# Kernel tuning notes

Hardware: AMD Instinct MI355X
Metric: run time of the kernel (lower is better)

Reference implementation:

```python
import jax, jax.numpy as jnp
import numpy as np

B, C, D, N, K = 2, 64, 3, 4096, 16
E = 2 * C      # edge-feature channels (128)
H = 2 * E      # expansion hidden channels (256)


def setup_inputs() -> dict:
    key = jax.random.key(0)
    ks = jax.random.split(key, 7)
    s1 = 1.0 / np.sqrt(E).astype(np.float32)
    s2 = 1.0 / np.sqrt(H).astype(np.float32)
    return {
        "x":  jax.random.normal(ks[0], (B, C, D, N), jnp.float32),
        "W1": jax.random.normal(ks[1], (H, E), jnp.float32) * s1,
        "b1": jax.random.normal(ks[2], (H,), jnp.float32) * s1,
        "W2": jax.random.normal(ks[3], (H, H), jnp.float32) * s2,
        "b2": jax.random.normal(ks[4], (H,), jnp.float32) * s2,
        "W3": jax.random.normal(ks[5], (C, H), jnp.float32) * s2,
        "b3": jax.random.normal(ks[6], (C,), jnp.float32) * s2,
    }


def _knn_idx(pc, k):
    """pc: (B, C, N). Returns (B, k, N) indices of k nearest neighbors
    (self excluded), matching KNN(ref=pc, query=pc) then idx[:, 1:, :]."""
    sq = jnp.sum(pc * pc, axis=1)                                  # (B, N)
    d2 = sq[:, :, None] - 2.0 * jnp.einsum('bcn,bcm->bnm', pc, pc) + sq[:, None, :]
    _, idx = jax.lax.top_k(-d2, k + 1)                             # (B, N, k+1) nearest-first
    return jnp.transpose(idx[:, :, 1:], (0, 2, 1))                 # drop self -> (B, k, N)


def reference(x, W1, b1, W2, b2, W3, b3):
    mean_pc = jnp.mean(x, axis=2)                                  # (B, C, N)
    idx = _knn_idx(mean_pc, K)                                     # (B, K, N), int32
    # grouping_operation: out[b,c,k,n] = mean_pc[b, c, idx[b,k,n]]
    nbr = jax.vmap(lambda f, i: f[:, i])(mean_pc, idx)             # (B, C, K, N)
    central = jnp.broadcast_to(x[:, :, None, :, :], (B, C, K, D, N))
    nbr_e = jnp.broadcast_to(nbr[:, :, :, None, :], (B, C, K, D, N))
    edge = jnp.concatenate([central, nbr_e - central], axis=1)     # (B, 2C, K, D, N)
    bc = lambda b: b[None, :, None, None, None]
    h = jax.nn.relu(jnp.einsum('oi,bikdn->bokdn', W1, edge) + bc(b1))
    h = jax.nn.relu(jnp.einsum('oi,bikdn->bokdn', W2, h) + bc(b2))
    r = jnp.einsum('oi,bikdn->bokdn', W3, h) + bc(b3)              # (B, C, K, D, N)
    return jnp.max(r, axis=2) + x                                  # (B, C, D, N)
```

## Files before the change

kernel.cpp:

```cpp
#include <hip/hip_runtime.h>

typedef unsigned short u16;
typedef float f32x4 __attribute__((ext_vector_type(4)));
typedef short bf16x8 __attribute__((ext_vector_type(8)));
typedef u16 u16x4 __attribute__((ext_vector_type(4)));
typedef unsigned int uint2v __attribute__((ext_vector_type(2)));


static __device__ __forceinline__ u16 f2bf(float x) {
    union { float f; unsigned int u; } v; v.f = x;
    unsigned int u = v.u;
    unsigned int r = u + 0x7fffu + ((u >> 16) & 1u);
    return (u16)(r >> 16);
}

static __device__ __forceinline__ float bf2f(u16 h) {
    union { unsigned int u; float f; } v; v.u = ((unsigned int)h) << 16;
    return v.f;
}

static __device__ __forceinline__ unsigned int pk2(float a, float b) {
    return (unsigned int)f2bf(a) | ((unsigned int)f2bf(b) << 16);
}

__global__ __launch_bounds__(256) void mean_kernel(const float* __restrict__ x,
                                                   float* __restrict__ pc,
                                                   const float* __restrict__ W1,
                                                   const float* __restrict__ W2,
                                                   const float* __restrict__ W3,
                                                   u16* __restrict__ W2bf,
                                                   u16* __restrict__ W3bf,
                                                   float* __restrict__ W1dT,
                                                   float* __restrict__ W1bT) {
    int t = blockIdx.x * 256 + threadIdx.x;
    int n = t & 4095;
    int bc = t >> 12;
    const float* xp = x + bc * 3 * 4096 + n;
    pc[t] = (xp[0] + xp[4096] + xp[8192]) / 3.0f;

    if (t < 65536) {
        W2bf[t] = f2bf(W2[t]);
        if (t < 16384) {
            W3bf[t] = f2bf(W3[t]);
            int c = t >> 8, h = t & 255;
            float wa = W1[h * 128 + c];
            float wb = W1[h * 128 + 64 + c];
            W1dT[t] = wa - wb;
            W1bT[t] = wb;
        }
    }
}

#define INSERT(dist, idxv) do { \
    float _v = (dist); int _vi = (idxv); \
    _Pragma("unroll") \
    for (int _s = 0; _s < 16; ++_s) { \
        bool _c = _v < bd[_s]; \
        float _nb = _c ? _v : bd[_s]; \
        float _nv = _c ? bd[_s] : _v; \
        int _nbi = _c ? _vi : bi[_s]; \
        int _nvi = _c ? bi[_s] : _vi; \
        bd[_s] = _nb; _v = _nv; bi[_s] = _nbi; _vi = _nvi; \
    } } while (0)

__global__ __launch_bounds__(256, 3) void knn_part_kernel(const float* __restrict__ pc,
                                                          float* __restrict__ pd,
                                                          int* __restrict__ pi) {
    __shared__ float ptile[64][128];
    __shared__ float sqt[128];
    int tid = threadIdx.x;
    int bid = blockIdx.x;
    int ch = bid & 31, qb = (bid >> 5) & 15, b = bid >> 9;
    int n = qb * 256 + tid;
    int m0 = ch * 128;

    #pragma unroll
    for (int it = 0; it < 8; ++it) {
        int lin4 = it * 256 + tid;
        int c = lin4 >> 5, mm4 = (lin4 & 31) * 4;
        *(float4*)&ptile[c][mm4] =
            *(const float4*)&pc[(b * 64 + c) * 4096 + m0 + mm4];
    }
    __syncthreads();
    if (tid < 128) {
        float s = 0.f;
        #pragma unroll
        for (int c = 0; c < 64; ++c) {
            float v = ptile[c][tid];
            s = fmaf(v, v, s);
        }
        sqt[tid] = s;
    }

    float qv[64];
    float sqn = 0.f;
    #pragma unroll
    for (int c = 0; c < 64; ++c) {
        qv[c] = pc[(b * 64 + c) * 4096 + n];
        sqn = fmaf(qv[c], qv[c], sqn);
    }

    float bd[16]; int bi[16];
    #pragma unroll
    for (int s = 0; s < 16; ++s) { bd[s] = 3.4e38f; bi[s] = -1; }
    __syncthreads();

    for (int mb = 0; mb < 128; mb += 4) {
        float d0 = 0.f, d1 = 0.f, d2 = 0.f, d3 = 0.f;
        #pragma unroll
        for (int c = 0; c < 64; ++c) {
            float4 pv = *(const float4*)&ptile[c][mb];
            float qc = qv[c];
            d0 = fmaf(qc, pv.x, d0);
            d1 = fmaf(qc, pv.y, d1);
            d2 = fmaf(qc, pv.z, d2);
            d3 = fmaf(qc, pv.w, d3);
        }
        int m = m0 + mb;
        float e0 = (sqn - 2.f * d0) + sqt[mb + 0]; if (m + 0 == n) e0 = 3.4e38f;
        float e1 = (sqn - 2.f * d1) + sqt[mb + 1]; if (m + 1 == n) e1 = 3.4e38f;
        float e2 = (sqn - 2.f * d2) + sqt[mb + 2]; if (m + 2 == n) e2 = 3.4e38f;
        float e3 = (sqn - 2.f * d3) + sqt[mb + 3]; if (m + 3 == n) e3 = 3.4e38f;
        INSERT(e0, m + 0);
        INSERT(e1, m + 1);
        INSERT(e2, m + 2);
        INSERT(e3, m + 3);
    }
    int base = ((b * 4096 + n) * 32 + ch) * 16;
    #pragma unroll
    for (int s = 0; s < 16; ++s) { pd[base + s] = bd[s]; pi[base + s] = bi[s]; }
}

__global__ __launch_bounds__(256) void knn_merge_kernel(const float* __restrict__ pd,
                                                        const int* __restrict__ pi,
                                                        int* __restrict__ idxw) {
    int tid = threadIdx.x;
    int lane = tid & 63;
    int q = blockIdx.x * 4 + (tid >> 6);
    int base = q * 512;

    float d[8]; int ix[8];
    #pragma unroll
    for (int j = 0; j < 8; ++j) {
        d[j] = pd[base + lane + 64 * j];
        ix[j] = pi[base + lane + 64 * j];
    }

    for (int e = 0; e < 16; ++e) {
        float lmd = d[0]; int lmi = ix[0];
        #pragma unroll
        for (int j = 1; j < 8; ++j) {
            bool c = d[j] < lmd;
            lmd = c ? d[j] : lmd;
            lmi = c ? ix[j] : lmi;
        }
        float wm = lmd;
        #pragma unroll
        for (int off = 32; off; off >>= 1)
            wm = fminf(wm, __shfl_xor(wm, off));
        unsigned long long msk = __ballot(lmd == wm);
        int L = (int)__ffsll(msk) - 1;
        int wmi = __shfl(lmi, L);
        if (lane == 0) idxw[q * 16 + e] = wmi;
        if (lane == L) {
            #pragma unroll
            for (int j = 0; j < 8; ++j)
                if (ix[j] == wmi) d[j] = 3.4e38f;
        }
    }
}

__global__ __launch_bounds__(256) void qp_kernel(const float* __restrict__ pc,
                                                 const float* __restrict__ x,
                                                 const float* __restrict__ W1bT,
                                                 const float* __restrict__ W1dT,
                                                 const float* __restrict__ b1,
                                                 u16* __restrict__ Qbf,
                                                 u16* __restrict__ Pbf) {
    int h = threadIdx.x;
    int bid = blockIdx.x;
    if (bid < 1024) {
        int b = bid >> 9, m0 = (bid & 511) * 8;
        float a0 = 0.f, a1 = 0.f, a2 = 0.f, a3 = 0.f;
        float a4 = 0.f, a5 = 0.f, a6 = 0.f, a7 = 0.f;
        for (int c = 0; c < 64; ++c) {
            float w = W1bT[c * 256 + h];
            const float* pr = pc + (b * 64 + c) * 4096 + m0;
            float4 p0 = *(const float4*)pr;
            float4 p1 = *(const float4*)(pr + 4);
            a0 = fmaf(w, p0.x, a0); a1 = fmaf(w, p0.y, a1);
            a2 = fmaf(w, p0.z, a2); a3 = fmaf(w, p0.w, a3);
            a4 = fmaf(w, p1.x, a4); a5 = fmaf(w, p1.y, a5);
            a6 = fmaf(w, p1.z, a6); a7 = fmaf(w, p1.w, a7);
        }
        int ob = (b * 4096 + m0) * 256 + h;
        Qbf[ob] = f2bf(a0); Qbf[ob + 256] = f2bf(a1);
        Qbf[ob + 512] = f2bf(a2); Qbf[ob + 768] = f2bf(a3);
        Qbf[ob + 1024] = f2bf(a4); Qbf[ob + 1280] = f2bf(a5);
        Qbf[ob + 1536] = f2bf(a6); Qbf[ob + 1792] = f2bf(a7);
    } else {
        int pb = bid - 1024;
        int b = pb / 1536;
        int rem = pb % 1536;
        int d = rem >> 9;
        int n0 = (rem & 511) * 8;
        float bias = b1[h];
        float a0 = bias, a1 = bias, a2 = bias, a3 = bias;
        float a4 = bias, a5 = bias, a6 = bias, a7 = bias;
        for (int c = 0; c < 64; ++c) {
            float w = W1dT[c * 256 + h];
            const float* xr = x + ((b * 64 + c) * 3 + d) * 4096 + n0;
            float4 x0 = *(const float4*)xr;
            float4 x1 = *(const float4*)(xr + 4);
            a0 = fmaf(w, x0.x, a0); a1 = fmaf(w, x0.y, a1);
            a2 = fmaf(w, x0.z, a2); a3 = fmaf(w, x0.w, a3);
            a4 = fmaf(w, x1.x, a4); a5 = fmaf(w, x1.y, a5);
            a6 = fmaf(w, x1.z, a6); a7 = fmaf(w, x1.w, a7);
        }
        int ob = ((b * 3 + d) * 4096 + n0) * 256 + h;
        Pbf[ob] = f2bf(a0); Pbf[ob + 256] = f2bf(a1);
        Pbf[ob + 512] = f2bf(a2); Pbf[ob + 768] = f2bf(a3);
        Pbf[ob + 1024] = f2bf(a4); Pbf[ob + 1280] = f2bf(a5);
        Pbf[ob + 1536] = f2bf(a6); Pbf[ob + 1792] = f2bf(a7);
    }
}

__global__ __launch_bounds__(512) void fused_mlp_kernel(const float* __restrict__ x,
                                                        const u16* __restrict__ Pbf,
                                                        const u16* __restrict__ Qbf,
                                                        const int* __restrict__ idxw,
                                                        const u16* __restrict__ W2bf,
                                                        const u16* __restrict__ W3bf,
                                                        const float* __restrict__ b2,
                                                        const float* __restrict__ b3,
                                                        float* __restrict__ out) {
    __shared__ u16 hL[96][264];

    int tid = threadIdx.x;
    int bid = blockIdx.x;
    int b = bid >> 11;
    int rr = bid & 2047;
    int n0 = (((rr & 7) << 8) | (rr >> 3)) << 1;

    int w = tid >> 6, lane = tid & 63;
    int cl = lane & 15, q = lane >> 4;

    {
        int g = w & 1, kh = (w >> 1) * 4;
        int n = n0 + g;
        u16x4 pv[3];
        #pragma unroll
        for (int d = 0; d < 3; ++d)
            pv[d] = *(const u16x4*)&Pbf[((b * 3 + d) * 4096 + n) * 256 + lane * 4];
        const int* idq = idxw + (b * 4096 + n) * 16 + kh;
        #pragma unroll
        for (int kk = 0; kk < 4; ++kk) {
            int m = idq[kk];
            u16x4 qv = *(const u16x4*)&Qbf[(b * 4096 + m) * 256 + lane * 4];
            float q0 = bf2f(qv[0]), q1 = bf2f(qv[1]), q2 = bf2f(qv[2]), q3 = bf2f(qv[3]);
            #pragma unroll
            for (int d = 0; d < 3; ++d) {
                uint2v hv;
                hv[0] = pk2(fmaxf(bf2f(pv[d][0]) + q0, 0.f), fmaxf(bf2f(pv[d][1]) + q1, 0.f));
                hv[1] = pk2(fmaxf(bf2f(pv[d][2]) + q2, 0.f), fmaxf(bf2f(pv[d][3]) + q3, 0.f));
                *(uint2v*)&hL[g * 48 + d * 16 + kh + kk][lane * 4] = hv;
            }
        }
    }
    __syncthreads();

    f32x4 acc[2][6];
    #pragma unroll
    for (int i = 0; i < 2; ++i)
        #pragma unroll
        for (int jt = 0; jt < 6; ++jt)
            acc[i][jt] = (f32x4){0.f, 0.f, 0.f, 0.f};

    const u16* Arow = W2bf + (w * 32 + cl) * 256 + q * 8;
    for (int kt = 0; kt < 8; ++kt) {
        int k0 = kt * 32;
        bf16x8 a[2], bb[6];
        #pragma unroll
        for (int i = 0; i < 2; ++i)
            a[i] = *(const bf16x8*)(Arow + i * 4096 + k0);
        #pragma unroll
        for (int jt = 0; jt < 6; ++jt)
            bb[jt] = *(const bf16x8*)(&hL[jt * 16 + cl][k0 + q * 8]);
        #pragma unroll
        for (int i = 0; i < 2; ++i)
            #pragma unroll
            for (int jt = 0; jt < 6; ++jt)
                acc[i][jt] = __builtin_amdgcn_mfma_f32_16x16x32_bf16(a[i], bb[jt], acc[i][jt], 0, 0, 0);
    }
    __syncthreads();

    #pragma unroll
    for (int i = 0; i < 2; ++i) {
        int rowb = w * 32 + i * 16 + q * 4;
        float4 bv = *(const float4*)(b2 + rowb);
        #pragma unroll
        for (int jt = 0; jt < 6; ++jt) {
            f32x4 v = acc[i][jt];
            uint2v hv;
            hv[0] = pk2(fmaxf(v[0] + bv.x, 0.f), fmaxf(v[1] + bv.y, 0.f));
            hv[1] = pk2(fmaxf(v[2] + bv.z, 0.f), fmaxf(v[3] + bv.w, 0.f));
            *(uint2v*)&hL[jt * 16 + cl][rowb] = hv;
        }
    }
    __syncthreads();

    int rw = (w & 3) * 16, jt0 = (w >> 2) * 3;
    f32x4 acc3[3];
    #pragma unroll
    for (int jt = 0; jt < 3; ++jt) acc3[jt] = (f32x4){0.f, 0.f, 0.f, 0.f};

    const u16* A3row = W3bf + (rw + cl) * 256 + q * 8;
    for (int kt = 0; kt < 8; ++kt) {
        int k0 = kt * 32;
        bf16x8 a3 = *(const bf16x8*)(A3row + k0);
        #pragma unroll
        for (int jt = 0; jt < 3; ++jt) {
            bf16x8 bb = *(const bf16x8*)(&hL[(jt0 + jt) * 16 + cl][k0 + q * 8]);
            acc3[jt] = __builtin_amdgcn_mfma_f32_16x16x32_bf16(a3, bb, acc3[jt], 0, 0, 0);
        }
    }

    int rowb = rw + q * 4;
    float4 b3v = *(const float4*)(b3 + rowb);
    #pragma unroll
    for (int jt = 0; jt < 3; ++jt) {
        int jj = jt0 + jt;
        int g = jj / 3, d = jj % 3;
        int n = n0 + g;
        f32x4 v = acc3[jt];
        v[0] += b3v.x;
        v[1] += b3v.y;
        v[2] += b3v.z;
        v[3] += b3v.w;
        #pragma unroll
        for (int off = 1; off < 16; off <<= 1) {
            v[0] = fmaxf(v[0], __shfl_xor(v[0], off));
            v[1] = fmaxf(v[1], __shfl_xor(v[1], off));
            v[2] = fmaxf(v[2], __shfl_xor(v[2], off));
            v[3] = fmaxf(v[3], __shfl_xor(v[3], off));
        }
        if (cl == 0) {
            #pragma unroll
            for (int r = 0; r < 4; ++r) {
                int addr = ((b * 64 + rowb + r) * 3 + d) * 4096 + n;
                out[addr] = v[r] + x[addr];
            }
        }
    }
}

extern "C" void kernel_launch(void* const* d_in, const int* in_sizes, int n_in,
                              void* d_out, int out_size, void* d_ws, size_t ws_size,
                              hipStream_t stream) {
    (void)in_sizes; (void)n_in; (void)out_size; (void)ws_size;
    const float* x  = (const float*)d_in[0];
    const float* W1 = (const float*)d_in[1];
    const float* b1 = (const float*)d_in[2];
    const float* W2 = (const float*)d_in[3];
    const float* b2 = (const float*)d_in[4];
    const float* W3 = (const float*)d_in[5];
    const float* b3 = (const float*)d_in[6];
    float* out = (float*)d_out;

    char* ws = (char*)d_ws;
    float* pc   = (float*)(ws + 0);
    int*   idxw = (int*)  (ws + 2129920);
    u16*   Qbf  = (u16*)  (ws + 2654208);
    u16*   Pbf  = (u16*)  (ws + 6848512);
    u16*   W2bf = (u16*)  (ws + 19431424);
    u16*   W3bf = (u16*)  (ws + 19562496);
    float* W1dT = (float*)(ws + 19595264);
    float* W1bT = (float*)(ws + 19660800);
    float* pd   = (float*)(ws + 2654208);
    int*   pi   = (int*)  (ws + 19726336);

    mean_kernel<<<2048, 256, 0, stream>>>(x, pc, W1, W2, W3, W2bf, W3bf, W1dT, W1bT);
    knn_part_kernel<<<1024, 256, 0, stream>>>(pc, pd, pi);
    knn_merge_kernel<<<2048, 256, 0, stream>>>(pd, pi, idxw);
    qp_kernel<<<4096, 256, 0, stream>>>(pc, x, W1bT, W1dT, b1, Qbf, Pbf);
    fused_mlp_kernel<<<4096, 512, 0, stream>>>(x, Pbf, Qbf, idxw, W2bf, W3bf, b2, b3, out);
}
```

Before: 338.0 us.

## Compute first-layer projections with bf16 MFMA and retile the second GEMM

Replaces the scalar FMA qp kernel with an MFMA-based bf16 kernel, with bf16 copies of x, the mean point cloud and the transposed W1 halves produced in the mean kernel. The KNN partial indices are stored as 16-bit to cut the partial-result traffic. The fused MLP's W2 GEMM is retiled from 2x6 to 4x3 MFMA tiles per wave, which changes the balance between A-operand global loads and B-operand LDS loads. Quantising x and pc to bf16 before the first layer adds rounding error, and the mean kernel now writes extra data.

```diff
diff --git a/kernel.cpp b/kernel.cpp
--- a/kernel.cpp
+++ b/kernel.cpp
@@ -30,13 +30,22 @@
                                                    const float* __restrict__ W3,
                                                    u16* __restrict__ W2bf,
                                                    u16* __restrict__ W3bf,
-                                                   float* __restrict__ W1dT,
-                                                   float* __restrict__ W1bT) {
+                                                   u16* __restrict__ W1dTbf,
+                                                   u16* __restrict__ W1bTbf,
+                                                   u16* __restrict__ xbf,
+                                                   u16* __restrict__ pcbf) {
     int t = blockIdx.x * 256 + threadIdx.x;
     int n = t & 4095;
     int bc = t >> 12;
     const float* xp = x + bc * 3 * 4096 + n;
-    pc[t] = (xp[0] + xp[4096] + xp[8192]) / 3.0f;
+    float x0 = xp[0], x1 = xp[4096], x2 = xp[8192];
+    float m = (x0 + x1 + x2) / 3.0f;
+    pc[t] = m;
+    pcbf[t] = f2bf(m);
+    int xb = bc * 3 * 4096 + n;
+    xbf[xb] = f2bf(x0);
+    xbf[xb + 4096] = f2bf(x1);
+    xbf[xb + 8192] = f2bf(x2);
 
     if (t < 65536) {
         W2bf[t] = f2bf(W2[t]);
@@ -45,8 +54,8 @@
             int c = t >> 8, h = t & 255;
             float wa = W1[h * 128 + c];
             float wb = W1[h * 128 + 64 + c];
-            W1dT[t] = wa - wb;
-            W1bT[t] = wb;
+            W1dTbf[h * 64 + c] = f2bf(wa - wb);
+            W1bTbf[h * 64 + c] = f2bf(wb);
         }
     }
 }
@@ -65,7 +74,7 @@
 
 __global__ __launch_bounds__(256, 3) void knn_part_kernel(const float* __restrict__ pc,
                                                           float* __restrict__ pd,
-                                                          int* __restrict__ pi) {
+                                                          u16* __restrict__ pi) {
     __shared__ float ptile[64][128];
     __shared__ float sqt[128];
     int tid = threadIdx.x;
@@ -102,7 +111,7 @@
 
     float bd[16]; int bi[16];
     #pragma unroll
-    for (int s = 0; s < 16; ++s) { bd[s] = 3.4e38f; bi[s] = -1; }
+    for (int s = 0; s < 16; ++s) { bd[s] = 3.4e38f; bi[s] = 0; }
     __syncthreads();
 
     for (int mb = 0; mb < 128; mb += 4) {
@@ -128,11 +137,11 @@
     }
     int base = ((b * 4096 + n) * 32 + ch) * 16;
     #pragma unroll
-    for (int s = 0; s < 16; ++s) { pd[base + s] = bd[s]; pi[base + s] = bi[s]; }
+    for (int s = 0; s < 16; ++s) { pd[base + s] = bd[s]; pi[base + s] = (u16)bi[s]; }
 }
 
 __global__ __launch_bounds__(256) void knn_merge_kernel(const float* __restrict__ pd,
-                                                        const int* __restrict__ pi,
+                                                        const u16* __restrict__ pi,
                                                         int* __restrict__ idxw) {
     int tid = threadIdx.x;
     int lane = tid & 63;
@@ -143,7 +152,7 @@
     #pragma unroll
     for (int j = 0; j < 8; ++j) {
         d[j] = pd[base + lane + 64 * j];
-        ix[j] = pi[base + lane + 64 * j];
+        ix[j] = (int)pi[base + lane + 64 * j];
     }
 
     for (int e = 0; e < 16; ++e) {
@@ -170,58 +179,69 @@
     }
 }
 
-__global__ __launch_bounds__(256) void qp_kernel(const float* __restrict__ pc,
-                                                 const float* __restrict__ x,
-                                                 const float* __restrict__ W1bT,
-                                                 const float* __restrict__ W1dT,
-                                                 const float* __restrict__ b1,
-                                                 u16* __restrict__ Qbf,
-                                                 u16* __restrict__ Pbf) {
-    int h = threadIdx.x;
-    int bid = blockIdx.x;
-    if (bid < 1024) {
-        int b = bid >> 9, m0 = (bid & 511) * 8;
-        float a0 = 0.f, a1 = 0.f, a2 = 0.f, a3 = 0.f;
-        float a4 = 0.f, a5 = 0.f, a6 = 0.f, a7 = 0.f;
-        for (int c = 0; c < 64; ++c) {
-            float w = W1bT[c * 256 + h];
-            const float* pr = pc + (b * 64 + c) * 4096 + m0;
-            float4 p0 = *(const float4*)pr;
-            float4 p1 = *(const float4*)(pr + 4);
-            a0 = fmaf(w, p0.x, a0); a1 = fmaf(w, p0.y, a1);
-            a2 = fmaf(w, p0.z, a2); a3 = fmaf(w, p0.w, a3);
-            a4 = fmaf(w, p1.x, a4); a5 = fmaf(w, p1.y, a5);
-            a6 = fmaf(w, p1.z, a6); a7 = fmaf(w, p1.w, a7);
-        }
-        int ob = (b * 4096 + m0) * 256 + h;
-        Qbf[ob] = f2bf(a0); Qbf[ob + 256] = f2bf(a1);
-        Qbf[ob + 512] = f2bf(a2); Qbf[ob + 768] = f2bf(a3);
-        Qbf[ob + 1024] = f2bf(a4); Qbf[ob + 1280] = f2bf(a5);
-        Qbf[ob + 1536] = f2bf(a6); Qbf[ob + 1792] = f2bf(a7);
+__global__ __launch_bounds__(256) void qp_mfma_kernel(const u16* __restrict__ xbf,
+                                                      const u16* __restrict__ pcbf,
+                                                      const u16* __restrict__ W1dTbf,
+                                                      const u16* __restrict__ W1bTbf,
+                                                      const float* __restrict__ b1,
+                                                      u16* __restrict__ Qbf,
+                                                      u16* __restrict__ Pbf) {
+    int tid = threadIdx.x, bid = blockIdx.x;
+    int w = tid >> 6, lane = tid & 63, cl = lane & 15, q = lane >> 4;
+
+    const u16* Wt;
+    const u16* src;
+    u16* dst;
+    int cstride;
+    bool isP;
+    if (bid < 128) {
+        int lin = bid * 64;
+        int b = lin >> 12, m0 = lin & 4095;
+        Wt = W1bTbf;
+        dst = Qbf + (b * 4096 + m0) * 256;
+        src = pcbf + b * 64 * 4096 + m0;
+        cstride = 4096;
+        isP = false;
     } else {
-        int pb = bid - 1024;
-        int b = pb / 1536;
-        int rem = pb % 1536;
-        int d = rem >> 9;
-        int n0 = (rem & 511) * 8;
-        float bias = b1[h];
-        float a0 = bias, a1 = bias, a2 = bias, a3 = bias;
-        float a4 = bias, a5 = bias, a6 = bias, a7 = bias;
-        for (int c = 0; c < 64; ++c) {
-            float w = W1dT[c * 256 + h];
-            const float* xr = x + ((b * 64 + c) * 3 + d) * 4096 + n0;
-            float4 x0 = *(const float4*)xr;
-            float4 x1 = *(const float4*)(xr + 4);
-            a0 = fmaf(w, x0.x, a0); a1 = fmaf(w, x0.y, a1);
-            a2 = fmaf(w, x0.z, a2); a3 = fmaf(w, x0.w, a3);
-            a4 = fmaf(w, x1.x, a4); a5 = fmaf(w, x1.y, a5);
-            a6 = fmaf(w, x1.z, a6); a7 = fmaf(w, x1.w, a7);
-        }
-        int ob = ((b * 3 + d) * 4096 + n0) * 256 + h;
-        Pbf[ob] = f2bf(a0); Pbf[ob + 256] = f2bf(a1);
-        Pbf[ob + 512] = f2bf(a2); Pbf[ob + 768] = f2bf(a3);
-        Pbf[ob + 1024] = f2bf(a4); Pbf[ob + 1280] = f2bf(a5);
-        Pbf[ob + 1536] = f2bf(a6); Pbf[ob + 1792] = f2bf(a7);
+        int lin = (bid - 128) * 64;
+        int b = lin / 12288;
+        int r = lin % 12288;
+        int d = r >> 12, n0 = r & 4095;
+        Wt = W1dTbf;
+        dst = Pbf + ((b * 3 + d) * 4096 + n0) * 256;
+        src = xbf + ((b * 64) * 3 + d) * 4096 + n0;
+        cstride = 3 * 4096;
+        isP = true;
+    }
+    int cw = w * 16;
+
+    bf16x8 bfr[2];
+    #pragma unroll
+    for (int kh = 0; kh < 2; ++kh)
+        #pragma unroll
+        for (int j = 0; j < 8; ++j) {
+            int c = kh * 32 + q * 8 + j;
+            bfr[kh][j] = (short)src[c * cstride + cw + cl];
+        }
+
+    #pragma unroll
+    for (int ht = 0; ht < 16; ++ht) {
+        f32x4 acc = (f32x4){0.f, 0.f, 0.f, 0.f};
+        const u16* arow = Wt + (ht * 16 + cl) * 64 + q * 8;
+        bf16x8 a0 = *(const bf16x8*)arow;
+        bf16x8 a1 = *(const bf16x8*)(arow + 32);
+        acc = __builtin_amdgcn_mfma_f32_16x16x32_bf16(a0, bfr[0], acc, 0, 0, 0);
+        acc = __builtin_amdgcn_mfma_f32_16x16x32_bf16(a1, bfr[1], acc, 0, 0, 0);
+        u16x4 o;
+        if (isP) {
+            float4 bv = *(const float4*)(b1 + ht * 16 + q * 4);
+            o[0] = f2bf(acc[0] + bv.x); o[1] = f2bf(acc[1] + bv.y);
+            o[2] = f2bf(acc[2] + bv.z); o[3] = f2bf(acc[3] + bv.w);
+        } else {
+            o[0] = f2bf(acc[0]); o[1] = f2bf(acc[1]);
+            o[2] = f2bf(acc[2]); o[3] = f2bf(acc[3]);
+        }
+        *(u16x4*)&dst[(cw + cl) * 256 + ht * 16 + q * 4] = o;
     }
 }
 
@@ -269,42 +289,43 @@
     }
     __syncthreads();
 
-    f32x4 acc[2][6];
-    #pragma unroll
-    for (int i = 0; i < 2; ++i)
-        #pragma unroll
-        for (int jt = 0; jt < 6; ++jt)
+    int rowg = w & 3, colh = w >> 2;
+    f32x4 acc[4][3];
+    #pragma unroll
+    for (int i = 0; i < 4; ++i)
+        #pragma unroll
+        for (int jt = 0; jt < 3; ++jt)
             acc[i][jt] = (f32x4){0.f, 0.f, 0.f, 0.f};
 
-    const u16* Arow = W2bf + (w * 32 + cl) * 256 + q * 8;
+    const u16* Arow = W2bf + (rowg * 64 + cl) * 256 + q * 8;
     for (int kt = 0; kt < 8; ++kt) {
         int k0 = kt * 32;
-        bf16x8 a[2], bb[6];
-        #pragma unroll
-        for (int i = 0; i < 2; ++i)
+        bf16x8 a[4], bb[3];
+        #pragma unroll
+        for (int i = 0; i < 4; ++i)
             a[i] = *(const bf16x8*)(Arow + i * 4096 + k0);
         #pragma unroll
-        for (int jt = 0; jt < 6; ++jt)
-            bb[jt] = *(const bf16x8*)(&hL[jt * 16 + cl][k0 + q * 8]);
-        #pragma unroll
-        for (int i = 0; i < 2; ++i)
+        for (int jt = 0; jt < 3; ++jt)
+            bb[jt] = *(const bf16x8*)(&hL[(colh * 3 + jt) * 16 + cl][k0 + q * 8]);
+        #pragma unroll
+        for (int i = 0; i < 4; ++i)
             #pragma unroll
-            for (int jt = 0; jt < 6; ++jt)
+            for (int jt = 0; jt < 3; ++jt)
                 acc[i][jt] = __builtin_amdgcn_mfma_f32_16x16x32_bf16(a[i], bb[jt], acc[i][jt], 0, 0, 0);
     }
     __syncthreads();
 
     #pragma unroll
-    for (int i = 0; i < 2; ++i) {
-        int rowb = w * 32 + i * 16 + q * 4;
+    for (int i = 0; i < 4; ++i) {
+        int rowb = rowg * 64 + i * 16 + q * 4;
         float4 bv = *(const float4*)(b2 + rowb);
         #pragma unroll
-        for (int jt = 0; jt < 6; ++jt) {
+        for (int jt = 0; jt < 3; ++jt) {
             f32x4 v = acc[i][jt];
             uint2v hv;
             hv[0] = pk2(fmaxf(v[0] + bv.x, 0.f), fmaxf(v[1] + bv.y, 0.f));
             hv[1] = pk2(fmaxf(v[2] + bv.z, 0.f), fmaxf(v[3] + bv.w, 0.f));
-            *(uint2v*)&hL[jt * 16 + cl][rowb] = hv;
+            *(uint2v*)&hL[(colh * 3 + jt) * 16 + cl][rowb] = hv;
         }
     }
     __syncthreads();
@@ -368,20 +389,23 @@
     float* out = (float*)d_out;
 
     char* ws = (char*)d_ws;
-    float* pc   = (float*)(ws + 0);
-    int*   idxw = (int*)  (ws + 2129920);
-    u16*   Qbf  = (u16*)  (ws + 2654208);
-    u16*   Pbf  = (u16*)  (ws + 6848512);
-    u16*   W2bf = (u16*)  (ws + 19431424);
-    u16*   W3bf = (u16*)  (ws + 19562496);
-    float* W1dT = (float*)(ws + 19595264);
-    float* W1bT = (float*)(ws + 19660800);
-    float* pd   = (float*)(ws + 2654208);
-    int*   pi   = (int*)  (ws + 19726336);
-
-    mean_kernel<<<2048, 256, 0, stream>>>(x, pc, W1, W2, W3, W2bf, W3bf, W1dT, W1bT);
+    float* pc     = (float*)(ws + 0);
+    int*   idxw   = (int*)  (ws + 2129920);
+    u16*   Qbf    = (u16*)  (ws + 2654208);
+    u16*   Pbf    = (u16*)  (ws + 6848512);
+    u16*   W2bf   = (u16*)  (ws + 19431424);
+    u16*   W3bf   = (u16*)  (ws + 19562496);
+    u16*   W1dTbf = (u16*)  (ws + 19595264);
+    u16*   W1bTbf = (u16*)  (ws + 19628032);
+    u16*   xbf    = (u16*)  (ws + 19660800);
+    u16*   pcbf   = (u16*)  (ws + 25952256);
+    float* pd     = (float*)(ws + 2654208);
+    u16*   pi     = (u16*)  (ws + 28049408);
+
+    mean_kernel<<<2048, 256, 0, stream>>>(x, pc, W1, W2, W3, W2bf, W3bf,
+                                          W1dTbf, W1bTbf, xbf, pcbf);
     knn_part_kernel<<<1024, 256, 0, stream>>>(pc, pd, pi);
     knn_merge_kernel<<<2048, 256, 0, stream>>>(pd, pi, idxw);
-    qp_kernel<<<4096, 256, 0, stream>>>(pc, x, W1bT, W1dT, b1, Qbf, Pbf);
+    qp_mfma_kernel<<<512, 256, 0, stream>>>(xbf, pcbf, W1dTbf, W1bTbf, b1, Qbf, Pbf);
     fused_mlp_kernel<<<4096, 512, 0, stream>>>(x, Pbf, Qbf, idxw, W2bf, W3bf, b2, b3, out);
 }
```

Result: slower. 384.1 us (+13.6%).
